# Kernel optimization log

Measured on AMD Instinct MI355X. Metric: run time of the kernel, lower is better.

Reference implementation:

```python
import jax, jax.numpy as jnp
import numpy as np

N = 50000      # nodes
E = 600000     # edges (avg degree 12)
IN, H, OUT = 128, 256, 256


def setup_inputs() -> dict:
    key = jax.random.key(0)
    ks = jax.random.split(key, 9)
    glorot = lambda k, shp: jax.random.uniform(
        k, shp, jnp.float32, -1.0, 1.0) * np.sqrt(6.0 / (shp[0] + shp[1]))
    return {
        "x": jax.random.normal(ks[0], (N, IN), jnp.float32),
        "src": jax.random.randint(ks[1], (E,), 0, N, jnp.int32),
        "dst": jax.random.randint(ks[2], (E,), 0, N, jnp.int32),
        "W_conv": glorot(ks[3], (IN, H)),
        "b_conv": jnp.zeros((H,), jnp.float32),
        "W_fc": glorot(ks[4], (H, H)),
        "b_fc": jax.random.uniform(ks[5], (H,), jnp.float32, -1, 1) / np.sqrt(H),
        "W_fc2": glorot(ks[6], (H, OUT)),
        "b_fc2": jax.random.uniform(ks[7], (OUT,), jnp.float32, -1, 1) / np.sqrt(OUT),
    }


def reference(x, src, dst, W_conv, b_conv, W_fc, b_fc, W_fc2, b_fc2):
    ones = jnp.ones((E,), x.dtype)
    # dgl GraphConv, norm='both': D_in^{-1/2} A D_out^{-1/2} X W + b
    deg_out = jax.ops.segment_sum(ones, src, num_segments=N)
    deg_in = jax.ops.segment_sum(ones, dst, num_segments=N)
    norm_src = jax.lax.rsqrt(jnp.maximum(deg_out, 1.0))  # [N]
    norm_dst = jax.lax.rsqrt(jnp.maximum(deg_in, 1.0))   # [N]
    feat = x * norm_src[:, None]                          # [N, IN]
    agg = jax.ops.segment_sum(feat[src], dst, num_segments=N)  # gather+scatter SpMM
    h = agg * norm_dst[:, None]
    h = h @ W_conv + b_conv                               # GraphConv weight+bias
    # num_nonl_layers == 2 branch
    h = jax.nn.relu(h) @ W_fc + b_fc
    h = jax.nn.relu(h) @ W_fc2 + b_fc2
    return h
```

## Files before the change

### kernel.cpp

```cpp
#include <hip/hip_runtime.h>

#define NN 50000
#define NE 600000
#define FIN 128
#define CAPS 128
#define CAPU 64
#define PW1 136
#define PW2 264

typedef __attribute__((ext_vector_type(8))) short bf16x8;
typedef __attribute__((ext_vector_type(4))) float f32x4;

__device__ __forceinline__ unsigned short f2bf(float f) {
    union { float f; unsigned int i; } v; v.f = f;
    return (unsigned short)((v.i + 0x7FFFu + ((v.i >> 16) & 1u)) >> 16);
}


__global__ __launch_bounds__(256)
void bin_kernel(const int* __restrict__ src, const int* __restrict__ dst,
                int* __restrict__ cnt_in, int* __restrict__ cnt_out,
                int* __restrict__ csr_src) {
    int e0 = (blockIdx.x * 256 + threadIdx.x) * 4;
    if (e0 >= NE) return;
    int4 s4 = *(const int4*)(src + e0);
    int4 d4 = *(const int4*)(dst + e0);
    int p;
    p = atomicAdd(&cnt_in[d4.x], 1); if (p < CAPU) csr_src[d4.x * CAPS + p] = s4.x;
    atomicAdd(&cnt_out[s4.x], 1);
    p = atomicAdd(&cnt_in[d4.y], 1); if (p < CAPU) csr_src[d4.y * CAPS + p] = s4.y;
    atomicAdd(&cnt_out[s4.y], 1);
    p = atomicAdd(&cnt_in[d4.z], 1); if (p < CAPU) csr_src[d4.z * CAPS + p] = s4.z;
    atomicAdd(&cnt_out[s4.z], 1);
    p = atomicAdd(&cnt_in[d4.w], 1); if (p < CAPU) csr_src[d4.w * CAPS + p] = s4.w;
    atomicAdd(&cnt_out[s4.w], 1);
}

__global__ __launch_bounds__(256)
void gather_kernel(const float* __restrict__ x, const int* __restrict__ csr_src,
                   const int* __restrict__ cnt_in, const int* __restrict__ cnt_out,
                   char* __restrict__ slotbase) {
    int tid  = threadIdx.x;
    int grp  = tid >> 5;
    int lane = tid & 31;
    int r = blockIdx.x * 8 + grp;
    if (r >= NN) return;
    int deg = cnt_in[r];
    float nd = rsqrtf(fmaxf((float)deg, 1.0f));
    int cnt = deg > CAPU ? CAPU : deg;
    const int* bucket = csr_src + (size_t)r * CAPS;
    const float* xb = x + lane * 4;
    float4 acc = {0.f, 0.f, 0.f, 0.f};
    for (int j0 = 0; j0 < cnt; j0 += 32) {
        int c = cnt - j0; if (c > 32) c = 32;
        int sv = 0; float nsl = 0.f;
        if (lane < c) {
            sv  = bucket[j0 + lane];
            nsl = rsqrtf(fmaxf((float)cnt_out[sv], 1.0f));
        }
        int i = 0;
        for (; i + 4 <= c; i += 4) {
            int   s0 = __shfl(sv, i, 32),     s1 = __shfl(sv, i + 1, 32);
            int   s2 = __shfl(sv, i + 2, 32), s3 = __shfl(sv, i + 3, 32);
            float n0 = __shfl(nsl, i, 32),     n1 = __shfl(nsl, i + 1, 32);
            float n2 = __shfl(nsl, i + 2, 32), n3 = __shfl(nsl, i + 3, 32);
            float4 v0 = *(const float4*)(xb + (size_t)s0 * FIN);
            float4 v1 = *(const float4*)(xb + (size_t)s1 * FIN);
            float4 v2 = *(const float4*)(xb + (size_t)s2 * FIN);
            float4 v3 = *(const float4*)(xb + (size_t)s3 * FIN);
            acc.x += v0.x * n0; acc.y += v0.y * n0; acc.z += v0.z * n0; acc.w += v0.w * n0;
            acc.x += v1.x * n1; acc.y += v1.y * n1; acc.z += v1.z * n1; acc.w += v1.w * n1;
            acc.x += v2.x * n2; acc.y += v2.y * n2; acc.z += v2.z * n2; acc.w += v2.w * n2;
            acc.x += v3.x * n3; acc.y += v3.y * n3; acc.z += v3.z * n3; acc.w += v3.w * n3;
        }
        for (; i < c; ++i) {
            int   s  = __shfl(sv,  i, 32);
            float ns = __shfl(nsl, i, 32);
            float4 xv = *(const float4*)(xb + (size_t)s * FIN);
            acc.x += xv.x * ns; acc.y += xv.y * ns;
            acc.z += xv.z * ns; acc.w += xv.w * ns;
        }
    }
    unsigned short o[4];
    o[0] = f2bf(acc.x * nd); o[1] = f2bf(acc.y * nd);
    o[2] = f2bf(acc.z * nd); o[3] = f2bf(acc.w * nd);
    *(uint2*)(slotbase + (size_t)r * 1024 + 768 + lane * 8) = *(const uint2*)o;
}

__global__ __launch_bounds__(256)
void wprep_kernel(const float* __restrict__ Wc, const float* __restrict__ W1,
                  const float* __restrict__ W2, unsigned short* __restrict__ o) {
    int t = blockIdx.x * 256 + threadIdx.x;
    if (t < 32768) {
        int n = t >> 7, k = t & 127;
        o[t] = f2bf(Wc[k * 256 + n]);
    } else if (t < 98304) {
        int i = t - 32768; int n = i >> 8, k = i & 255;
        o[32768 + i] = f2bf(W1[k * 256 + n]);
    } else if (t < 163840) {
        int i = t - 98304; int n = i >> 8, k = i & 255;
        o[98304 + i] = f2bf(W2[k * 256 + n]);
    }
}

__global__ __launch_bounds__(256)
void gemm1_kernel(char* slotbase, const unsigned short* __restrict__ Wct,
                  const float* __restrict__ bc) {
    __shared__ short wsh[64 * PW1];
    int tid = threadIdx.x;
    int wave = tid >> 6, lane = tid & 63;
    int quad = lane >> 4, l16 = lane & 15;
    int m0 = blockIdx.x * 64 + wave * 16;
    int arow = m0 + l16; if (arow >= NN) arow = NN - 1;
    const unsigned short* Ap =
        (const unsigned short*)(slotbase + (size_t)arow * 1024 + 768) + quad * 8;
    bf16x8 a[4];
    #pragma unroll
    for (int i = 0; i < 4; ++i) a[i] = *(const bf16x8*)(Ap + i * 32);
    int sc = tid >> 2, sq = tid & 3;
    #pragma unroll 1
    for (int p = 0; p < 4; ++p) {
        __syncthreads();
        {
            const unsigned short* g = Wct + (size_t)(p * 64 + sc) * 128 + sq * 32;
            #pragma unroll
            for (int j = 0; j < 4; ++j)
                *(bf16x8*)&wsh[sc * PW1 + sq * 32 + j * 8] = *(const bf16x8*)(g + j * 8);
        }
        __syncthreads();
        f32x4 ac0 = {0.f,0.f,0.f,0.f}, ac1 = ac0, ac2 = ac0, ac3 = ac0;
        #pragma unroll
        for (int i = 0; i < 4; ++i) {
            int k0 = i * 32;
            bf16x8 b0 = *(const bf16x8*)&wsh[( 0 + l16) * PW1 + quad * 8 + k0];
            bf16x8 b1 = *(const bf16x8*)&wsh[(16 + l16) * PW1 + quad * 8 + k0];
            bf16x8 b2 = *(const bf16x8*)&wsh[(32 + l16) * PW1 + quad * 8 + k0];
            bf16x8 b3 = *(const bf16x8*)&wsh[(48 + l16) * PW1 + quad * 8 + k0];
            ac0 = __builtin_amdgcn_mfma_f32_16x16x32_bf16(a[i], b0, ac0, 0, 0, 0);
            ac1 = __builtin_amdgcn_mfma_f32_16x16x32_bf16(a[i], b1, ac1, 0, 0, 0);
            ac2 = __builtin_amdgcn_mfma_f32_16x16x32_bf16(a[i], b2, ac2, 0, 0, 0);
            ac3 = __builtin_amdgcn_mfma_f32_16x16x32_bf16(a[i], b3, ac3, 0, 0, 0);
        }
        int n0 = p * 64;
        f32x4 accs[4] = {ac0, ac1, ac2, ac3};
        #pragma unroll
        for (int c = 0; c < 4; ++c) {
            int col = n0 + c * 16 + l16;
            float bv = bc[col];
            #pragma unroll
            for (int r2 = 0; r2 < 4; ++r2) {
                int rr = m0 + quad * 4 + r2;
                if (rr < NN)
                    *(unsigned short*)(slotbase + (size_t)rr * 1024 + 512 + 2 * col) =
                        f2bf(fmaxf(accs[c][r2] + bv, 0.0f));
            }
        }
    }
}

template<bool FINAL>
__global__ __launch_bounds__(256)
void gemm23_kernel(char* slotbase, const unsigned short* __restrict__ Wt,
                   const float* __restrict__ bias) {
    __shared__ short wsh[64 * PW2];
    int tid = threadIdx.x;
    int wave = tid >> 6, lane = tid & 63;
    int quad = lane >> 4, l16 = lane & 15;
    int m0 = blockIdx.x * 64 + wave * 16;
    int arow = m0 + l16; if (arow >= NN) arow = NN - 1;
    const unsigned short* Ap =
        (const unsigned short*)(slotbase + (size_t)arow * 1024 + (FINAL ? 0 : 512)) + quad * 8;
    bf16x8 a[8];
    #pragma unroll
    for (int i = 0; i < 8; ++i) a[i] = *(const bf16x8*)(Ap + i * 32);
    int sc = tid >> 2, sq = tid & 3;
    #pragma unroll 1
    for (int p = 0; p < 4; ++p) {
        __syncthreads();
        {
            const unsigned short* g = Wt + (size_t)(p * 64 + sc) * 256 + sq * 64;
            #pragma unroll
            for (int j = 0; j < 8; ++j)
                *(bf16x8*)&wsh[sc * PW2 + sq * 64 + j * 8] = *(const bf16x8*)(g + j * 8);
        }
        __syncthreads();
        f32x4 ac0 = {0.f,0.f,0.f,0.f}, ac1 = ac0, ac2 = ac0, ac3 = ac0;
        #pragma unroll
        for (int i = 0; i < 8; ++i) {
            int k0 = i * 32;
            bf16x8 b0 = *(const bf16x8*)&wsh[( 0 + l16) * PW2 + quad * 8 + k0];
            bf16x8 b1 = *(const bf16x8*)&wsh[(16 + l16) * PW2 + quad * 8 + k0];
            bf16x8 b2 = *(const bf16x8*)&wsh[(32 + l16) * PW2 + quad * 8 + k0];
            bf16x8 b3 = *(const bf16x8*)&wsh[(48 + l16) * PW2 + quad * 8 + k0];
            ac0 = __builtin_amdgcn_mfma_f32_16x16x32_bf16(a[i], b0, ac0, 0, 0, 0);
            ac1 = __builtin_amdgcn_mfma_f32_16x16x32_bf16(a[i], b1, ac1, 0, 0, 0);
            ac2 = __builtin_amdgcn_mfma_f32_16x16x32_bf16(a[i], b2, ac2, 0, 0, 0);
            ac3 = __builtin_amdgcn_mfma_f32_16x16x32_bf16(a[i], b3, ac3, 0, 0, 0);
        }
        int n0 = p * 64;
        f32x4 accs[4] = {ac0, ac1, ac2, ac3};
        #pragma unroll
        for (int c = 0; c < 4; ++c) {
            int col = n0 + c * 16 + l16;
            float bv = bias[col];
            #pragma unroll
            for (int r2 = 0; r2 < 4; ++r2) {
                int rr = m0 + quad * 4 + r2;
                if (rr < NN) {
                    float v = accs[c][r2] + bv;
                    if (FINAL)
                        *(float*)(slotbase + (size_t)rr * 1024 + 4 * col) = v;
                    else
                        *(unsigned short*)(slotbase + (size_t)rr * 1024 + 2 * col) =
                            f2bf(fmaxf(v, 0.0f));
                }
            }
        }
    }
}


extern "C" void kernel_launch(void* const* d_in, const int* in_sizes, int n_in,
                              void* d_out, int out_size, void* d_ws, size_t ws_size,
                              hipStream_t stream) {
    const float* x      = (const float*)d_in[0];
    const int*   src    = (const int*)d_in[1];
    const int*   dst    = (const int*)d_in[2];
    const float* W_conv = (const float*)d_in[3];
    const float* b_conv = (const float*)d_in[4];
    const float* W_fc   = (const float*)d_in[5];
    const float* b_fc   = (const float*)d_in[6];
    const float* W_fc2  = (const float*)d_in[7];
    const float* b_fc2  = (const float*)d_in[8];
    char* slotbase = (char*)d_out;

    int* csr_src = (int*)(slotbase + 16000000);

    char* ws = (char*)d_ws;
    int* cnt_out = (int*)(ws + 0);
    int* cnt_in  = (int*)(ws + 204800);
    unsigned short* Wct = (unsigned short*)(ws + 0);
    unsigned short* W1t = (unsigned short*)(ws + 65536);
    unsigned short* W2t = (unsigned short*)(ws + 196608);

    hipMemsetAsync(d_ws, 0, 409600, stream);

    bin_kernel<<<(NE / 4 + 255) / 256, 256, 0, stream>>>(src, dst, cnt_in, cnt_out,
                                                         csr_src);
    gather_kernel<<<(NN + 7) / 8, 256, 0, stream>>>(x, csr_src, cnt_in, cnt_out,
                                                    slotbase);
    wprep_kernel<<<640, 256, 0, stream>>>(W_conv, W_fc, W_fc2, (unsigned short*)ws);

    int nb = (NN + 63) / 64;
    gemm1_kernel<<<nb, 256, 0, stream>>>(slotbase, Wct, b_conv);
    gemm23_kernel<false><<<nb, 256, 0, stream>>>(slotbase, W1t, b_fc);
    gemm23_kernel<true ><<<nb, 256, 0, stream>>>(slotbase, W2t, b_fc2);
}
```

Measured before the change: 269.2 us.

## Double rows per wave in GEMM kernels and use one edge per thread in binning

```diff
diff --git a/kernel.cpp b/kernel.cpp
--- a/kernel.cpp
+++ b/kernel.cpp
@@ -21,19 +21,13 @@
 void bin_kernel(const int* __restrict__ src, const int* __restrict__ dst,
                 int* __restrict__ cnt_in, int* __restrict__ cnt_out,
                 int* __restrict__ csr_src) {
-    int e0 = (blockIdx.x * 256 + threadIdx.x) * 4;
-    if (e0 >= NE) return;
-    int4 s4 = *(const int4*)(src + e0);
-    int4 d4 = *(const int4*)(dst + e0);
-    int p;
-    p = atomicAdd(&cnt_in[d4.x], 1); if (p < CAPU) csr_src[d4.x * CAPS + p] = s4.x;
-    atomicAdd(&cnt_out[s4.x], 1);
-    p = atomicAdd(&cnt_in[d4.y], 1); if (p < CAPU) csr_src[d4.y * CAPS + p] = s4.y;
-    atomicAdd(&cnt_out[s4.y], 1);
-    p = atomicAdd(&cnt_in[d4.z], 1); if (p < CAPU) csr_src[d4.z * CAPS + p] = s4.z;
-    atomicAdd(&cnt_out[s4.z], 1);
-    p = atomicAdd(&cnt_in[d4.w], 1); if (p < CAPU) csr_src[d4.w * CAPS + p] = s4.w;
-    atomicAdd(&cnt_out[s4.w], 1);
+    int e = blockIdx.x * 256 + threadIdx.x;
+    if (e < NE) {
+        int s = src[e], d = dst[e];
+        int p = atomicAdd(&cnt_in[d], 1);
+        if (p < CAPU) csr_src[d * CAPS + p] = s;
+        atomicAdd(&cnt_out[s], 1);
+    }
 }
 
 __global__ __launch_bounds__(256)
@@ -110,13 +104,16 @@
     int tid = threadIdx.x;
     int wave = tid >> 6, lane = tid & 63;
     int quad = lane >> 4, l16 = lane & 15;
-    int m0 = blockIdx.x * 64 + wave * 16;
-    int arow = m0 + l16; if (arow >= NN) arow = NN - 1;
-    const unsigned short* Ap =
-        (const unsigned short*)(slotbase + (size_t)arow * 1024 + 768) + quad * 8;
-    bf16x8 a[4];
+    int m0 = blockIdx.x * 128 + wave * 32;
+    bf16x8 a[2][4];
     #pragma unroll
-    for (int i = 0; i < 4; ++i) a[i] = *(const bf16x8*)(Ap + i * 32);
+    for (int g = 0; g < 2; ++g) {
+        int arow = m0 + g * 16 + l16; if (arow >= NN) arow = NN - 1;
+        const unsigned short* Ap =
+            (const unsigned short*)(slotbase + (size_t)arow * 1024 + 768) + quad * 8;
+        #pragma unroll
+        for (int i = 0; i < 4; ++i) a[g][i] = *(const bf16x8*)(Ap + i * 32);
+    }
     int sc = tid >> 2, sq = tid & 3;
     #pragma unroll 1
     for (int p = 0; p < 4; ++p) {
@@ -128,7 +125,7 @@
                 *(bf16x8*)&wsh[sc * PW1 + sq * 32 + j * 8] = *(const bf16x8*)(g + j * 8);
         }
         __syncthreads();
-        f32x4 ac0 = {0.f,0.f,0.f,0.f}, ac1 = ac0, ac2 = ac0, ac3 = ac0;
+        f32x4 acc[2][4] = {};
         #pragma unroll
         for (int i = 0; i < 4; ++i) {
             int k0 = i * 32;
@@ -136,23 +133,28 @@
             bf16x8 b1 = *(const bf16x8*)&wsh[(16 + l16) * PW1 + quad * 8 + k0];
             bf16x8 b2 = *(const bf16x8*)&wsh[(32 + l16) * PW1 + quad * 8 + k0];
             bf16x8 b3 = *(const bf16x8*)&wsh[(48 + l16) * PW1 + quad * 8 + k0];
-            ac0 = __builtin_amdgcn_mfma_f32_16x16x32_bf16(a[i], b0, ac0, 0, 0, 0);
-            ac1 = __builtin_amdgcn_mfma_f32_16x16x32_bf16(a[i], b1, ac1, 0, 0, 0);
-            ac2 = __builtin_amdgcn_mfma_f32_16x16x32_bf16(a[i], b2, ac2, 0, 0, 0);
-            ac3 = __builtin_amdgcn_mfma_f32_16x16x32_bf16(a[i], b3, ac3, 0, 0, 0);
+            #pragma unroll
+            for (int g = 0; g < 2; ++g) {
+                acc[g][0] = __builtin_amdgcn_mfma_f32_16x16x32_bf16(a[g][i], b0, acc[g][0], 0, 0, 0);
+                acc[g][1] = __builtin_amdgcn_mfma_f32_16x16x32_bf16(a[g][i], b1, acc[g][1], 0, 0, 0);
+                acc[g][2] = __builtin_amdgcn_mfma_f32_16x16x32_bf16(a[g][i], b2, acc[g][2], 0, 0, 0);
+                acc[g][3] = __builtin_amdgcn_mfma_f32_16x16x32_bf16(a[g][i], b3, acc[g][3], 0, 0, 0);
+            }
         }
         int n0 = p * 64;
-        f32x4 accs[4] = {ac0, ac1, ac2, ac3};
         #pragma unroll
         for (int c = 0; c < 4; ++c) {
             int col = n0 + c * 16 + l16;
             float bv = bc[col];
             #pragma unroll
-            for (int r2 = 0; r2 < 4; ++r2) {
-                int rr = m0 + quad * 4 + r2;
-                if (rr < NN)
-                    *(unsigned short*)(slotbase + (size_t)rr * 1024 + 512 + 2 * col) =
-                        f2bf(fmaxf(accs[c][r2] + bv, 0.0f));
+            for (int g = 0; g < 2; ++g) {
+                #pragma unroll
+                for (int r2 = 0; r2 < 4; ++r2) {
+                    int rr = m0 + g * 16 + quad * 4 + r2;
+                    if (rr < NN)
+                        *(unsigned short*)(slotbase + (size_t)rr * 1024 + 512 + 2 * col) =
+                            f2bf(fmaxf(acc[g][c][r2] + bv, 0.0f));
+                }
             }
         }
     }
@@ -166,13 +168,16 @@
     int tid = threadIdx.x;
     int wave = tid >> 6, lane = tid & 63;
     int quad = lane >> 4, l16 = lane & 15;
-    int m0 = blockIdx.x * 64 + wave * 16;
-    int arow = m0 + l16; if (arow >= NN) arow = NN - 1;
-    const unsigned short* Ap =
-        (const unsigned short*)(slotbase + (size_t)arow * 1024 + (FINAL ? 0 : 512)) + quad * 8;
-    bf16x8 a[8];
+    int m0 = blockIdx.x * 128 + wave * 32;
+    bf16x8 a[2][8];
     #pragma unroll
-    for (int i = 0; i < 8; ++i) a[i] = *(const bf16x8*)(Ap + i * 32);
+    for (int g = 0; g < 2; ++g) {
+        int arow = m0 + g * 16 + l16; if (arow >= NN) arow = NN - 1;
+        const unsigned short* Ap =
+            (const unsigned short*)(slotbase + (size_t)arow * 1024 + (FINAL ? 0 : 512)) + quad * 8;
+        #pragma unroll
+        for (int i = 0; i < 8; ++i) a[g][i] = *(const bf16x8*)(Ap + i * 32);
+    }
     int sc = tid >> 2, sq = tid & 3;
     #pragma unroll 1
     for (int p = 0; p < 4; ++p) {
@@ -184,7 +189,7 @@
                 *(bf16x8*)&wsh[sc * PW2 + sq * 64 + j * 8] = *(const bf16x8*)(g + j * 8);
         }
         __syncthreads();
-        f32x4 ac0 = {0.f,0.f,0.f,0.f}, ac1 = ac0, ac2 = ac0, ac3 = ac0;
+        f32x4 acc[2][4] = {};
         #pragma unroll
         for (int i = 0; i < 8; ++i) {
             int k0 = i * 32;
@@ -192,27 +197,32 @@
             bf16x8 b1 = *(const bf16x8*)&wsh[(16 + l16) * PW2 + quad * 8 + k0];
             bf16x8 b2 = *(const bf16x8*)&wsh[(32 + l16) * PW2 + quad * 8 + k0];
             bf16x8 b3 = *(const bf16x8*)&wsh[(48 + l16) * PW2 + quad * 8 + k0];
-            ac0 = __builtin_amdgcn_mfma_f32_16x16x32_bf16(a[i], b0, ac0, 0, 0, 0);
-            ac1 = __builtin_amdgcn_mfma_f32_16x16x32_bf16(a[i], b1, ac1, 0, 0, 0);
-            ac2 = __builtin_amdgcn_mfma_f32_16x16x32_bf16(a[i], b2, ac2, 0, 0, 0);
-            ac3 = __builtin_amdgcn_mfma_f32_16x16x32_bf16(a[i], b3, ac3, 0, 0, 0);
+            #pragma unroll
+            for (int g = 0; g < 2; ++g) {
+                acc[g][0] = __builtin_amdgcn_mfma_f32_16x16x32_bf16(a[g][i], b0, acc[g][0], 0, 0, 0);
+                acc[g][1] = __builtin_amdgcn_mfma_f32_16x16x32_bf16(a[g][i], b1, acc[g][1], 0, 0, 0);
+                acc[g][2] = __builtin_amdgcn_mfma_f32_16x16x32_bf16(a[g][i], b2, acc[g][2], 0, 0, 0);
+                acc[g][3] = __builtin_amdgcn_mfma_f32_16x16x32_bf16(a[g][i], b3, acc[g][3], 0, 0, 0);
+            }
         }
         int n0 = p * 64;
-        f32x4 accs[4] = {ac0, ac1, ac2, ac3};
         #pragma unroll
         for (int c = 0; c < 4; ++c) {
             int col = n0 + c * 16 + l16;
             float bv = bias[col];
             #pragma unroll
-            for (int r2 = 0; r2 < 4; ++r2) {
-                int rr = m0 + quad * 4 + r2;
-                if (rr < NN) {
-                    float v = accs[c][r2] + bv;
-                    if (FINAL)
-                        *(float*)(slotbase + (size_t)rr * 1024 + 4 * col) = v;
-                    else
-                        *(unsigned short*)(slotbase + (size_t)rr * 1024 + 2 * col) =
-                            f2bf(fmaxf(v, 0.0f));
+            for (int g = 0; g < 2; ++g) {
+                #pragma unroll
+                for (int r2 = 0; r2 < 4; ++r2) {
+                    int rr = m0 + g * 16 + quad * 4 + r2;
+                    if (rr < NN) {
+                        float v = acc[g][c][r2] + bv;
+                        if (FINAL)
+                            *(float*)(slotbase + (size_t)rr * 1024 + 4 * col) = v;
+                        else
+                            *(unsigned short*)(slotbase + (size_t)rr * 1024 + 2 * col) =
+                                f2bf(fmaxf(v, 0.0f));
+                    }
                 }
             }
         }
@@ -245,13 +255,13 @@
 
     hipMemsetAsync(d_ws, 0, 409600, stream);
 
-    bin_kernel<<<(NE / 4 + 255) / 256, 256, 0, stream>>>(src, dst, cnt_in, cnt_out,
-                                                         csr_src);
+    bin_kernel<<<(NE + 255) / 256, 256, 0, stream>>>(src, dst, cnt_in, cnt_out,
+                                                     csr_src);
     gather_kernel<<<(NN + 7) / 8, 256, 0, stream>>>(x, csr_src, cnt_in, cnt_out,
                                                     slotbase);
     wprep_kernel<<<640, 256, 0, stream>>>(W_conv, W_fc, W_fc2, (unsigned short*)ws);
 
-    int nb = (NN + 63) / 64;
+    int nb = (NN + 127) / 128;
     gemm1_kernel<<<nb, 256, 0, stream>>>(slotbase, Wct, b_conv);
     gemm23_kernel<false><<<nb, 256, 0, stream>>>(slotbase, W1t, b_fc);
     gemm23_kernel<true ><<<nb, 256, 0, stream>>>(slotbase, W2t, b_fc2);
```

Result: slower. 274.6 us (+2.0%).
